# Kernel tuning notes

Hardware: AMD Instinct MI355X
Metric: run time of the kernel (lower is better)

## Reference

```python
import jax, jax.numpy as jnp
import numpy as np

N_NODES = 100000
N_SUPPORTS = 3
N_EDGES = 500000
D_IN = 128
D_OUT = 128


def setup_inputs() -> dict:
    key = jax.random.key(0)
    k1, k2, k3, k4, k5 = jax.random.split(key, 5)
    x = jax.random.normal(k1, (N_NODES, D_IN), dtype=jnp.float32)
    # glorot-ish scale for weights
    W = jax.random.normal(k2, (N_SUPPORTS, D_IN, D_OUT), dtype=jnp.float32) * np.sqrt(2.0 / (D_IN + D_OUT)).astype(np.float32)
    edge_src = jax.random.randint(k3, (N_SUPPORTS, N_EDGES), 0, N_NODES, dtype=jnp.int32)
    edge_dst = jax.random.randint(k4, (N_SUPPORTS, N_EDGES), 0, N_NODES, dtype=jnp.int32)
    edge_val = jax.random.uniform(k5, (N_SUPPORTS, N_EDGES), dtype=jnp.float32)
    return {"x": x, "W": W, "edge_src": edge_src, "edge_dst": edge_dst, "edge_val": edge_val}


def reference(x, W, edge_src, edge_dst, edge_val):
    """HMGConvolution forward (adj_power=1, multi_weight, no attention/reweight).

    x:        [N, Din] dense node features
    W:        [S, Din, Dout] per-support weights
    edge_src: [S, E] source node ids of each adjacency (COO)
    edge_dst: [S, E] destination node ids
    edge_val: [S, E] adjacency values
    Returns relu(sum_s  A_s @ (x @ W_s))  -> [N, Dout]
    """
    n_nodes = x.shape[0]
    # dense transform per support: [S, N, Dout]
    pre_sup = jnp.einsum('nd,sde->sne', x, W)

    def spmm(pre_s, src, dst, val):
        # messages gathered from source nodes, scaled by edge weight
        msgs = val[:, None] * pre_s[src]  # [E, Dout]
        return jax.ops.segment_sum(msgs, dst, num_segments=n_nodes)  # [N, Dout]

    supports = jax.vmap(spmm)(pre_sup, edge_src, edge_dst, edge_val)  # [S, N, Dout]
    return jax.nn.relu(jnp.sum(supports, axis=0))
```

## Files before the change

### kernel.cpp

```cpp
#include <hip/hip_runtime.h>

#define DIN 128
#define DOUT 128
#define EPB 4096
#define BKT 512
#define PACK_BITS 19
#define SRCG_MASK ((1u << PACK_BITS) - 1u)

typedef __attribute__((ext_vector_type(8))) short short8;
typedef __attribute__((ext_vector_type(4))) float f32x4;
typedef __attribute__((ext_vector_type(8))) unsigned short ushort8;

__device__ __forceinline__ unsigned short f2bf(float f) {
  unsigned int u = __float_as_uint(f);
  u += 0x7fffu + ((u >> 16) & 1u);
  return (unsigned short)(u >> 16);
}


__global__ __launch_bounds__(256) void gemm_mfma(const float* __restrict__ x,
                                                 const float* __restrict__ W,
                                                 unsigned short* __restrict__ pre,
                                                 int n_nodes, int n_sup) {
  __shared__ unsigned short xs[128][136];
  __shared__ unsigned short wt[128][136];

  const int tid = threadIdx.x;
  const int lane = tid & 63;
  const int w = tid >> 6;
  const int row0 = blockIdx.x * 128;
  const int alr = lane & 15;
  const int akg = lane >> 4;

#pragma unroll
  for (int i = 0; i < 16; ++i) {
    int e = tid + i * 256;
    int r = e >> 5;
    int c = (e & 31) * 4;
    int gr = row0 + r;
    float4 v = make_float4(0.f, 0.f, 0.f, 0.f);
    if (gr < n_nodes) v = *reinterpret_cast<const float4*>(&x[(size_t)gr * DIN + c]);
    xs[r][c] = f2bf(v.x); xs[r][c + 1] = f2bf(v.y);
    xs[r][c + 2] = f2bf(v.z); xs[r][c + 3] = f2bf(v.w);
  }
  __syncthreads();

  short8 afrag[4][2];
#pragma unroll
  for (int kc = 0; kc < 4; ++kc)
#pragma unroll
    for (int mt = 0; mt < 2; ++mt)
      afrag[kc][mt] = *reinterpret_cast<const short8*>(
          &xs[w * 32 + mt * 16 + alr][kc * 32 + akg * 8]);

  for (int s = 0; s < n_sup; ++s) {
    const float* Ws = W + (size_t)s * DIN * DOUT;
    __syncthreads();
#pragma unroll
    for (int i = 0; i < 16; ++i) {
      int e = tid + i * 256;
      int k = e >> 5;
      int c = (e & 31) * 4;
      float4 v = *reinterpret_cast<const float4*>(&Ws[(size_t)k * DOUT + c]);
      wt[c][k] = f2bf(v.x); wt[c + 1][k] = f2bf(v.y);
      wt[c + 2][k] = f2bf(v.z); wt[c + 3][k] = f2bf(v.w);
    }
    __syncthreads();

    f32x4 acc[2][8];
#pragma unroll
    for (int mt = 0; mt < 2; ++mt)
#pragma unroll
      for (int nt = 0; nt < 8; ++nt) acc[mt][nt] = (f32x4){0.f, 0.f, 0.f, 0.f};

#pragma unroll
    for (int kc = 0; kc < 4; ++kc) {
      short8 bfrag[8];
#pragma unroll
      for (int nt = 0; nt < 8; ++nt)
        bfrag[nt] = *reinterpret_cast<const short8*>(
            &wt[nt * 16 + alr][kc * 32 + akg * 8]);
#pragma unroll
      for (int mt = 0; mt < 2; ++mt)
#pragma unroll
        for (int nt = 0; nt < 8; ++nt)
          acc[mt][nt] = __builtin_amdgcn_mfma_f32_16x16x32_bf16(
              afrag[kc][mt], bfrag[nt], acc[mt][nt], 0, 0, 0);
    }
    __syncthreads();

#pragma unroll
    for (int mt = 0; mt < 2; ++mt)
#pragma unroll
      for (int nt = 0; nt < 8; ++nt)
#pragma unroll
        for (int q = 0; q < 4; ++q)
          wt[w * 32 + mt * 16 + akg * 4 + q][nt * 16 + alr] = f2bf(acc[mt][nt][q]);
    __syncthreads();

    unsigned short* ps = pre + (size_t)s * n_nodes * DOUT;
#pragma unroll
    for (int i = 0; i < 8; ++i) {
      int e = tid + i * 256;
      int r = e >> 4;
      int c = (e & 15) * 8;
      int gr = row0 + r;
      if (gr < n_nodes)
        *reinterpret_cast<ushort8*>(&ps[(size_t)gr * DOUT + c]) =
            *reinterpret_cast<const ushort8*>(&wt[r][c]);
    }
  }
}


__global__ __launch_bounds__(256) void gemm_xw(const float* __restrict__ x,
                                               const float* __restrict__ W,
                                               float* __restrict__ pre,
                                               int n_nodes) {
  __shared__ float xsf[128][33];
  __shared__ float wtf[32][129];
  const float* Ws = W + (size_t)blockIdx.y * DIN * DOUT;
  float* pres = pre + (size_t)blockIdx.y * n_nodes * DOUT;
  const int tid = threadIdx.x;
  const int row0 = blockIdx.x * 128;
  const int tcol = tid & 15;
  const int trow = tid >> 4;
  float acc[8][8];
#pragma unroll
  for (int i = 0; i < 8; ++i)
#pragma unroll
    for (int j = 0; j < 8; ++j) acc[i][j] = 0.f;
#pragma unroll 1
  for (int kk = 0; kk < DIN; kk += 32) {
#pragma unroll
    for (int i = 0; i < 4; ++i) {
      int e = tid + i * 256;
      int r = e >> 3, c = (e & 7) * 4;
      int gr = row0 + r;
      float4 v = make_float4(0.f, 0.f, 0.f, 0.f);
      if (gr < n_nodes)
        v = *reinterpret_cast<const float4*>(&x[(size_t)gr * DIN + kk + c]);
      xsf[r][c] = v.x; xsf[r][c + 1] = v.y; xsf[r][c + 2] = v.z; xsf[r][c + 3] = v.w;
    }
#pragma unroll
    for (int i = 0; i < 4; ++i) {
      int e = tid + i * 256;
      int k = e >> 5, c = (e & 31) * 4;
      float4 v = *reinterpret_cast<const float4*>(&Ws[(size_t)(kk + k) * DOUT + c]);
      wtf[k][c] = v.x; wtf[k][c + 1] = v.y; wtf[k][c + 2] = v.z; wtf[k][c + 3] = v.w;
    }
    __syncthreads();
#pragma unroll 4
    for (int k = 0; k < 32; ++k) {
      float a[8], b[8];
#pragma unroll
      for (int i = 0; i < 8; ++i) a[i] = xsf[trow * 8 + i][k];
#pragma unroll
      for (int j = 0; j < 8; ++j) b[j] = wtf[k][tcol + 16 * j];
#pragma unroll
      for (int i = 0; i < 8; ++i)
#pragma unroll
        for (int j = 0; j < 8; ++j) acc[i][j] = fmaf(a[i], b[j], acc[i][j]);
    }
    __syncthreads();
  }
#pragma unroll
  for (int i = 0; i < 8; ++i) {
    int gr = row0 + trow * 8 + i;
    if (gr < n_nodes) {
#pragma unroll
      for (int j = 0; j < 8; ++j)
        pres[(size_t)gr * DOUT + tcol + 16 * j] = acc[i][j];
    }
  }
}


__global__ __launch_bounds__(256) void bucket_count(const int* __restrict__ dst_all,
                                                    int* __restrict__ bucket_cnt, int TE) {
  __shared__ int cnt[256];
  const int tid = threadIdx.x;
  cnt[tid] = 0;
  __syncthreads();
  const int beg = blockIdx.x * EPB;
  const int end = min(beg + EPB, TE);
  for (int i = beg + tid; i < end; i += 256) atomicAdd(&cnt[dst_all[i] >> 9], 1);
  __syncthreads();
  int c = cnt[tid];
  if (c) atomicAdd(&bucket_cnt[tid], c);
}

__global__ __launch_bounds__(256) void bucket_scan(const int* __restrict__ bucket_cnt,
                                                   int* __restrict__ bucket_base,
                                                   int* __restrict__ bucket_cursor,
                                                   int NB, int TE) {
  __shared__ int tmp[256];
  const int tid = threadIdx.x;
  int v = (tid < NB) ? bucket_cnt[tid] : 0;
  tmp[tid] = v;
  __syncthreads();
#pragma unroll
  for (int d = 1; d < 256; d <<= 1) {
    int t = (tid >= d) ? tmp[tid - d] : 0;
    __syncthreads();
    tmp[tid] += t;
    __syncthreads();
  }
  int excl = tmp[tid] - v;
  if (tid < NB) {
    bucket_base[tid] = excl;
    bucket_cursor[tid] = excl;
  }
  if (tid == 0) bucket_base[NB] = TE;
}

__global__ __launch_bounds__(256) void partition_edges(const int* __restrict__ src_all,
                                                       const int* __restrict__ dst_all,
                                                       const float* __restrict__ val_all,
                                                       int* __restrict__ bucket_cursor,
                                                       int2* __restrict__ part,
                                                       int TE, int n_nodes, int n_edges) {
  __shared__ int cnt[256];
  __shared__ int base_l[256];
  const int tid = threadIdx.x;
  const int beg = blockIdx.x * EPB;
  const int end = min(beg + EPB, TE);

  cnt[tid] = 0;
  __syncthreads();
  for (int i = beg + tid; i < end; i += 256) atomicAdd(&cnt[dst_all[i] >> 9], 1);
  __syncthreads();

  int c = cnt[tid];
  int mybase = (c > 0) ? atomicAdd(&bucket_cursor[tid], c) : 0;
  __syncthreads();
  base_l[tid] = mybase;
  cnt[tid] = 0;
  __syncthreads();

  for (int i = beg + tid; i < end; i += 256) {
    int d = dst_all[i];
    int b = d >> 9;
    int r = atomicAdd(&cnt[b], 1);
    int s = i / n_edges;
    unsigned key = (unsigned)(s * n_nodes + src_all[i]) |
                   ((unsigned)(d & (BKT - 1)) << PACK_BITS);
    part[base_l[b] + r] = make_int2((int)key, __float_as_int(val_all[i]));
  }
}

__global__ __launch_bounds__(256) void csr_build(const int2* __restrict__ part,
                                                 const int* __restrict__ bucket_base,
                                                 int2* __restrict__ csr,
                                                 int* __restrict__ row_off,
                                                 int n_nodes, int TE) {
  __shared__ int cnt[BKT];
  __shared__ int off_s[BKT];
  __shared__ int tmp[256];
  const int b = blockIdx.x;
  const int tid = threadIdx.x;
  const int bb = bucket_base[b];
  const int be = bucket_base[b + 1];

  cnt[tid] = 0;
  cnt[tid + 256] = 0;
  __syncthreads();
  for (int j = bb + tid; j < be; j += 256)
    atomicAdd(&cnt[((unsigned)part[j].x) >> PACK_BITS], 1);
  __syncthreads();

  int s2 = cnt[2 * tid] + cnt[2 * tid + 1];
  tmp[tid] = s2;
  __syncthreads();
#pragma unroll
  for (int d = 1; d < 256; d <<= 1) {
    int t = (tid >= d) ? tmp[tid - d] : 0;
    __syncthreads();
    tmp[tid] += t;
    __syncthreads();
  }
  int excl2 = tmp[tid] - s2;
  off_s[2 * tid] = excl2;
  off_s[2 * tid + 1] = excl2 + cnt[2 * tid];
  __syncthreads();

#pragma unroll
  for (int k = tid; k < BKT; k += 256) {
    int node = b * BKT + k;
    if (node < n_nodes) row_off[node] = bb + off_s[k];
  }
  cnt[tid] = off_s[tid];
  cnt[tid + 256] = off_s[tid + 256];
  __syncthreads();

  for (int j = bb + tid; j < be; j += 256) {
    int2 e = part[j];
    int dl = ((unsigned)e.x) >> PACK_BITS;
    int p = bb + atomicAdd(&cnt[dl], 1);
    csr[p] = e;
  }
  if (b == 0 && tid == 0) row_off[n_nodes] = TE;
}


__global__ __launch_bounds__(256) void spmm_gather8(const unsigned short* __restrict__ pre,
                                                    const int2* __restrict__ csr,
                                                    const int* __restrict__ row_off,
                                                    float* __restrict__ out, int n_nodes) {
  const int lane = threadIdx.x & 63;
  const int g = lane >> 3;
  const int t = lane & 7;
  const int wave = blockIdx.x * (blockDim.x >> 6) + (threadIdx.x >> 6);
  const int nwaves = gridDim.x * (blockDim.x >> 6);

  for (int n = wave; n < n_nodes; n += nwaves) {
    const int beg = row_off[n];
    const int end = row_off[n + 1];
    float acc[16];
#pragma unroll
    for (int k = 0; k < 16; ++k) acc[k] = 0.f;

    for (int j = beg + g; j < end; j += 8) {
      const int2 e = csr[j];
      const float v = __int_as_float(e.y);
      const unsigned srcg = ((unsigned)e.x) & SRCG_MASK;
      const ushort8* pr =
          reinterpret_cast<const ushort8*>(&pre[(size_t)srcg * DOUT + t * 16]);
      ushort8 p0 = pr[0];
      ushort8 p1 = pr[1];
#pragma unroll
      for (int k = 0; k < 8; ++k) {
        acc[k]     = fmaf(v, __uint_as_float((unsigned int)(unsigned short)p0[k] << 16), acc[k]);
        acc[8 + k] = fmaf(v, __uint_as_float((unsigned int)(unsigned short)p1[k] << 16), acc[8 + k]);
      }
    }

#pragma unroll
    for (int d = 8; d <= 32; d <<= 1)
#pragma unroll
      for (int k = 0; k < 16; ++k) acc[k] += __shfl_xor(acc[k], d, 64);

    float r0 = 0.f, r1 = 0.f;
#pragma unroll
    for (int gg = 0; gg < 8; ++gg)
      if (gg == g) { r0 = acc[gg * 2]; r1 = acc[gg * 2 + 1]; }
    r0 = fmaxf(r0, 0.f);
    r1 = fmaxf(r1, 0.f);
    *reinterpret_cast<float2*>(&out[(size_t)n * DOUT + t * 16 + g * 2]) =
        make_float2(r0, r1);
  }
}


__global__ __launch_bounds__(256) void edge_hist(const int* __restrict__ dst_base,
                                                 int* __restrict__ counts,
                                                 int n_edges, int n_nodes) {
  int i = blockIdx.x * blockDim.x + threadIdx.x;
  int s = blockIdx.y;
  if (i < n_edges) atomicAdd(&counts[s * n_nodes + dst_base[(size_t)s * n_edges + i]], 1);
}

__global__ __launch_bounds__(256) void scan_local(const int* __restrict__ counts,
                                                  int* __restrict__ row_off,
                                                  int* __restrict__ partials, int n) {
  __shared__ int tmp[256];
  const int tid = threadIdx.x;
  const int base = blockIdx.x * 2048 + tid * 8;
  int v[8];
#pragma unroll
  for (int i = 0; i < 8; ++i) v[i] = (base + i < n) ? counts[base + i] : 0;
  int s = 0;
#pragma unroll
  for (int i = 0; i < 8; ++i) s += v[i];
  tmp[tid] = s;
  __syncthreads();
#pragma unroll
  for (int d = 1; d < 256; d <<= 1) {
    int t = (tid >= d) ? tmp[tid - d] : 0;
    __syncthreads();
    tmp[tid] += t;
    __syncthreads();
  }
  int p = tmp[tid] - s;
#pragma unroll
  for (int i = 0; i < 8; ++i) {
    if (base + i < n) row_off[base + i] = p;
    p += v[i];
  }
  if (tid == 255) partials[blockIdx.x] = tmp[255];
}

__global__ __launch_bounds__(256) void scan_partials_k(int* __restrict__ partials, int nblk) {
  __shared__ int tmp[256];
  const int tid = threadIdx.x;
  int v = (tid < nblk) ? partials[tid] : 0;
  tmp[tid] = v;
  __syncthreads();
#pragma unroll
  for (int d = 1; d < 256; d <<= 1) {
    int t = (tid >= d) ? tmp[tid - d] : 0;
    __syncthreads();
    tmp[tid] += t;
    __syncthreads();
  }
  if (tid < nblk) partials[tid] = tmp[tid] - v;
}

__global__ __launch_bounds__(256) void scan_finish(int* __restrict__ row_off,
                                                   int* __restrict__ cursor,
                                                   const int* __restrict__ partials,
                                                   int n, int total_edges) {
  const int off = partials[blockIdx.x];
  const int base = blockIdx.x * 2048 + threadIdx.x * 8;
#pragma unroll
  for (int i = 0; i < 8; ++i) {
    int idx = base + i;
    if (idx < n) {
      int v = row_off[idx] + off;
      row_off[idx] = v;
      cursor[idx] = v;
    }
  }
  if (blockIdx.x == 0 && threadIdx.x == 0) row_off[n] = total_edges;
}

__global__ __launch_bounds__(256) void edge_fill(const int* __restrict__ src_base,
                                                 const int* __restrict__ dst_base,
                                                 const float* __restrict__ val_base,
                                                 int* __restrict__ cursor,
                                                 int2* __restrict__ csr,
                                                 int n_edges, int n_nodes) {
  int i = blockIdx.x * blockDim.x + threadIdx.x;
  int s = blockIdx.y;
  if (i < n_edges) {
    size_t gi = (size_t)s * n_edges + i;
    int d = dst_base[gi];
    int pos = atomicAdd(&cursor[s * n_nodes + d], 1);
    csr[pos] = make_int2(src_base[gi], __float_as_int(val_base[gi]));
  }
}

__global__ __launch_bounds__(256) void spmm_gather(const float* __restrict__ pre,
                                                   const int2* __restrict__ csr,
                                                   const int* __restrict__ row_off,
                                                   float* __restrict__ out,
                                                   int n_nodes, int n_sup, int mode) {
  const int lane = threadIdx.x & 63;
  const int wave = blockIdx.x * (blockDim.x >> 6) + (threadIdx.x >> 6);
  const int nwaves = gridDim.x * (blockDim.x >> 6);
  for (int n = wave; n < n_nodes; n += nwaves) {
    float ax = 0.f, ay = 0.f;
    float2* o = reinterpret_cast<float2*>(&out[(size_t)n * DOUT + lane * 2]);
    if (mode & 1) { float2 prev = *o; ax = prev.x; ay = prev.y; }
    for (int s = 0; s < n_sup; ++s) {
      const float* ps = pre + (size_t)s * n_nodes * DOUT;
      const int row = s * n_nodes + n;
      const int beg = row_off[row];
      const int end = row_off[row + 1];
      for (int j = beg; j < end; ++j) {
        const int2 e = csr[j];
        const float v = __int_as_float(e.y);
        const float2 p = *reinterpret_cast<const float2*>(&ps[(size_t)e.x * DOUT + lane * 2]);
        ax = fmaf(v, p.x, ax);
        ay = fmaf(v, p.y, ay);
      }
    }
    if (mode & 2) { ax = fmaxf(ax, 0.f); ay = fmaxf(ay, 0.f); }
    *o = make_float2(ax, ay);
  }
}

__global__ __launch_bounds__(256) void zero_f4(float4* __restrict__ p, int n4) {
  int i = blockIdx.x * blockDim.x + threadIdx.x;
  int stride = gridDim.x * blockDim.x;
  float4 z = make_float4(0.f, 0.f, 0.f, 0.f);
  for (; i < n4; i += stride) p[i] = z;
}

__global__ __launch_bounds__(256) void relu_f4(float4* __restrict__ p, int n4) {
  int i = blockIdx.x * blockDim.x + threadIdx.x;
  int stride = gridDim.x * blockDim.x;
  for (; i < n4; i += stride) {
    float4 v = p[i];
    v.x = fmaxf(v.x, 0.f); v.y = fmaxf(v.y, 0.f);
    v.z = fmaxf(v.z, 0.f); v.w = fmaxf(v.w, 0.f);
    p[i] = v;
  }
}

__global__ __launch_bounds__(256) void spmm_atomic(const float* __restrict__ pre,
                                                   const int* __restrict__ src,
                                                   const int* __restrict__ dst,
                                                   const float* __restrict__ val,
                                                   float* __restrict__ out,
                                                   int n_edges) {
  const int lane = threadIdx.x & 63;
  const int wave = blockIdx.x * (blockDim.x >> 6) + (threadIdx.x >> 6);
  const int nwaves = gridDim.x * (blockDim.x >> 6);
  for (int e = wave; e < n_edges; e += nwaves) {
    int s = src[e];
    int d = dst[e];
    float v = val[e];
    const float2 p = *reinterpret_cast<const float2*>(&pre[(size_t)s * DOUT + lane * 2]);
    float* o = &out[(size_t)d * DOUT + lane * 2];
    atomicAdd(o, v * p.x);
    atomicAdd(o + 1, v * p.y);
  }
}


static inline size_t align_up(size_t v, size_t a) { return (v + a - 1) & ~(a - 1); }

extern "C" void kernel_launch(void* const* d_in, const int* in_sizes, int n_in,
                              void* d_out, int out_size, void* d_ws, size_t ws_size,
                              hipStream_t stream) {
  const float* x     = (const float*)d_in[0];
  const float* W     = (const float*)d_in[1];
  const int*   esrc  = (const int*)d_in[2];
  const int*   edst  = (const int*)d_in[3];
  const float* eval_ = (const float*)d_in[4];
  float* out = (float*)d_out;

  const int n_nodes    = in_sizes[0] / DIN;
  const int n_supports = in_sizes[1] / (DIN * DOUT);
  const int n_edges    = in_sizes[2] / n_supports;

  const int gemm_blocks = (n_nodes + 127) / 128;
  const int edge_blocks = (n_edges + 255) / 256;
  const int gather_blocks = (n_nodes + 3) / 4;

  {
    const int NR = n_supports * n_nodes;
    const int TE = n_supports * n_edges;
    const int NB = (n_nodes + BKT - 1) / BKT;
    const int eb = (TE + EPB - 1) / EPB;
    char* w = (char*)d_ws;
    size_t off = 0;
    unsigned short* pre3 = (unsigned short*)(w + off); off += align_up((size_t)NR * DOUT * 2, 256);
    int* row_off = (int*)(w + off);      off += align_up((size_t)(n_nodes + 1) * 4, 256);
    int2* part = (int2*)(w + off);       off += align_up((size_t)TE * 8, 256);
    int2* csr = (int2*)(w + off);        off += align_up((size_t)TE * 8, 256);
    int* bucket_cnt = (int*)(w + off);   off += align_up(256 * 4, 256);
    int* bucket_base = (int*)(w + off);  off += align_up(257 * 4, 256);
    int* bucket_cur = (int*)(w + off);   off += align_up(256 * 4, 256);

    const bool packable = (size_t)n_supports * n_nodes < (1u << PACK_BITS);

    if (off <= ws_size && NB <= 256 && packable) {
      gemm_mfma<<<gemm_blocks, 256, 0, stream>>>(x, W, pre3, n_nodes, n_supports);
      hipMemsetAsync(bucket_cnt, 0, 256 * 4, stream);
      bucket_count<<<eb, 256, 0, stream>>>(edst, bucket_cnt, TE);
      bucket_scan<<<1, 256, 0, stream>>>(bucket_cnt, bucket_base, bucket_cur, NB, TE);
      partition_edges<<<eb, 256, 0, stream>>>(esrc, edst, eval_, bucket_cur, part,
                                              TE, n_nodes, n_edges);
      csr_build<<<NB, 256, 0, stream>>>(part, bucket_base, csr, row_off, n_nodes, TE);
      spmm_gather8<<<gather_blocks, 256, 0, stream>>>(pre3, csr, row_off, out, n_nodes);
      return;
    }
  }

  {
    const int scan_blocks = (n_nodes + 2047) / 2048;
    char* w = (char*)d_ws;
    size_t off = 0;
    float* pre = (float*)(w + off);    off += align_up((size_t)n_nodes * DOUT * 4, 256);
    int* row_off = (int*)(w + off);    off += align_up((size_t)(n_nodes + 1) * 4, 256);
    int* cursor = (int*)(w + off);     off += align_up((size_t)n_nodes * 4, 256);
    int2* csr = (int2*)(w + off);      off += align_up((size_t)n_edges * 8, 256);
    int* partials = (int*)(w + off);   off += align_up(1024 * 4, 256);

    if (off <= ws_size && scan_blocks <= 256) {
      for (int s = 0; s < n_supports; ++s) {
        const int* src = esrc + (size_t)s * n_edges;
        const int* dst = edst + (size_t)s * n_edges;
        const float* val = eval_ + (size_t)s * n_edges;
        gemm_xw<<<dim3(gemm_blocks, 1), 256, 0, stream>>>(x, W + (size_t)s * DIN * DOUT,
                                                          pre, n_nodes);
        hipMemsetAsync(cursor, 0, (size_t)n_nodes * 4, stream);
        edge_hist<<<dim3(edge_blocks, 1), 256, 0, stream>>>(dst, cursor, n_edges, n_nodes);
        scan_local<<<scan_blocks, 256, 0, stream>>>(cursor, row_off, partials, n_nodes);
        scan_partials_k<<<1, 256, 0, stream>>>(partials, scan_blocks);
        scan_finish<<<scan_blocks, 256, 0, stream>>>(row_off, cursor, partials, n_nodes, n_edges);
        edge_fill<<<dim3(edge_blocks, 1), 256, 0, stream>>>(src, dst, val, cursor, csr,
                                                            n_edges, n_nodes);
        int mode = (s == 0) ? 0 : 1;
        if (s == n_supports - 1) mode |= 2;
        spmm_gather<<<gather_blocks, 256, 0, stream>>>(pre, csr, row_off, out,
                                                       n_nodes, 1, mode);
      }
      return;
    }
  }

  {
    float* pre = (float*)d_ws;
    if (ws_size < (size_t)n_nodes * DOUT * 4) return;
    const int n4 = out_size / 4;
    zero_f4<<<2048, 256, 0, stream>>>((float4*)out, n4);
    for (int s = 0; s < n_supports; ++s) {
      gemm_xw<<<dim3(gemm_blocks, 1), 256, 0, stream>>>(x, W + (size_t)s * DIN * DOUT,
                                                        pre, n_nodes);
      spmm_atomic<<<2048, 256, 0, stream>>>(pre, esrc + (size_t)s * n_edges,
                                            edst + (size_t)s * n_edges,
                                            eval_ + (size_t)s * n_edges, out, n_edges);
    }
    relu_f4<<<2048, 256, 0, stream>>>((float4*)out, n4);
  }
}
```

Baseline: 200.3 us.

## Pre-convert W to transposed bf16 once and load GEMM fragments from global

A new small kernel converts each support's weight matrix to bf16 and transposes it once, so GEMM blocks no longer convert and transpose W into shared memory for every support. The GEMM now builds its A fragments straight from global fp32 x in registers and reads B fragments from the pre-transposed bf16 buffer in global memory (served from cache). This removes the per-block shared staging, most barriers, and one LDS buffer, which may raise occupancy. In exchange it adds an extra kernel launch and relies on L2/L1 hits for repeated B fragment loads.

```diff
diff --git a/kernel.cpp b/kernel.cpp
--- a/kernel.cpp
+++ b/kernel.cpp
@@ -18,12 +18,37 @@
 }
 
 
+__global__ __launch_bounds__(256) void wconvert(const float* __restrict__ W,
+                                                unsigned short* __restrict__ wT) {
+  __shared__ unsigned short buf[128][136];
+  const int s = blockIdx.x;
+  const float* Ws = W + (size_t)s * DIN * DOUT;
+  unsigned short* wts = wT + (size_t)s * DIN * DOUT;
+  const int tid = threadIdx.x;
+#pragma unroll
+  for (int i = 0; i < 16; ++i) {
+    int e = tid + i * 256;
+    int k = e >> 5, c = (e & 31) * 4;
+    float4 v = *reinterpret_cast<const float4*>(&Ws[(size_t)k * DOUT + c]);
+    buf[c][k] = f2bf(v.x); buf[c + 1][k] = f2bf(v.y);
+    buf[c + 2][k] = f2bf(v.z); buf[c + 3][k] = f2bf(v.w);
+  }
+  __syncthreads();
+#pragma unroll
+  for (int i = 0; i < 8; ++i) {
+    int e = tid + i * 256;
+    int r = e >> 4, c = (e & 15) * 8;
+    *reinterpret_cast<ushort8*>(&wts[(size_t)r * DIN + c]) =
+        *reinterpret_cast<const ushort8*>(&buf[r][c]);
+  }
+}
+
+
 __global__ __launch_bounds__(256) void gemm_mfma(const float* __restrict__ x,
-                                                 const float* __restrict__ W,
+                                                 const unsigned short* __restrict__ wT,
                                                  unsigned short* __restrict__ pre,
                                                  int n_nodes, int n_sup) {
-  __shared__ unsigned short xs[128][136];
-  __shared__ unsigned short wt[128][136];
+  __shared__ unsigned short cst[128][136];
 
   const int tid = threadIdx.x;
   const int lane = tid & 63;
@@ -32,40 +57,28 @@
   const int alr = lane & 15;
   const int akg = lane >> 4;
 
-#pragma unroll
-  for (int i = 0; i < 16; ++i) {
-    int e = tid + i * 256;
-    int r = e >> 5;
-    int c = (e & 31) * 4;
-    int gr = row0 + r;
-    float4 v = make_float4(0.f, 0.f, 0.f, 0.f);
-    if (gr < n_nodes) v = *reinterpret_cast<const float4*>(&x[(size_t)gr * DIN + c]);
-    xs[r][c] = f2bf(v.x); xs[r][c + 1] = f2bf(v.y);
-    xs[r][c + 2] = f2bf(v.z); xs[r][c + 3] = f2bf(v.w);
-  }
-  __syncthreads();
-
   short8 afrag[4][2];
 #pragma unroll
   for (int kc = 0; kc < 4; ++kc)
 #pragma unroll
-    for (int mt = 0; mt < 2; ++mt)
-      afrag[kc][mt] = *reinterpret_cast<const short8*>(
-          &xs[w * 32 + mt * 16 + alr][kc * 32 + akg * 8]);
+    for (int mt = 0; mt < 2; ++mt) {
+      int gr = row0 + w * 32 + mt * 16 + alr;
+      short8 a = {0, 0, 0, 0, 0, 0, 0, 0};
+      if (gr < n_nodes) {
+        const float4* p =
+            reinterpret_cast<const float4*>(&x[(size_t)gr * DIN + kc * 32 + akg * 8]);
+        float4 v0 = p[0];
+        float4 v1 = p[1];
+        a[0] = (short)f2bf(v0.x); a[1] = (short)f2bf(v0.y);
+        a[2] = (short)f2bf(v0.z); a[3] = (short)f2bf(v0.w);
+        a[4] = (short)f2bf(v1.x); a[5] = (short)f2bf(v1.y);
+        a[6] = (short)f2bf(v1.z); a[7] = (short)f2bf(v1.w);
+      }
+      afrag[kc][mt] = a;
+    }
 
   for (int s = 0; s < n_sup; ++s) {
-    const float* Ws = W + (size_t)s * DIN * DOUT;
-    __syncthreads();
-#pragma unroll
-    for (int i = 0; i < 16; ++i) {
-      int e = tid + i * 256;
-      int k = e >> 5;
-      int c = (e & 31) * 4;
-      float4 v = *reinterpret_cast<const float4*>(&Ws[(size_t)k * DOUT + c]);
-      wt[c][k] = f2bf(v.x); wt[c + 1][k] = f2bf(v.y);
-      wt[c + 2][k] = f2bf(v.z); wt[c + 3][k] = f2bf(v.w);
-    }
-    __syncthreads();
+    const unsigned short* wts = wT + (size_t)s * DIN * DOUT;
 
     f32x4 acc[2][8];
 #pragma unroll
@@ -79,7 +92,7 @@
 #pragma unroll
       for (int nt = 0; nt < 8; ++nt)
         bfrag[nt] = *reinterpret_cast<const short8*>(
-            &wt[nt * 16 + alr][kc * 32 + akg * 8]);
+            &wts[(size_t)(nt * 16 + alr) * DIN + kc * 32 + akg * 8]);
 #pragma unroll
       for (int mt = 0; mt < 2; ++mt)
 #pragma unroll
@@ -87,15 +100,15 @@
           acc[mt][nt] = __builtin_amdgcn_mfma_f32_16x16x32_bf16(
               afrag[kc][mt], bfrag[nt], acc[mt][nt], 0, 0, 0);
     }
-    __syncthreads();
-
+
+    __syncthreads();
 #pragma unroll
     for (int mt = 0; mt < 2; ++mt)
 #pragma unroll
       for (int nt = 0; nt < 8; ++nt)
 #pragma unroll
         for (int q = 0; q < 4; ++q)
-          wt[w * 32 + mt * 16 + akg * 4 + q][nt * 16 + alr] = f2bf(acc[mt][nt][q]);
+          cst[w * 32 + mt * 16 + akg * 4 + q][nt * 16 + alr] = f2bf(acc[mt][nt][q]);
     __syncthreads();
 
     unsigned short* ps = pre + (size_t)s * n_nodes * DOUT;
@@ -107,7 +120,7 @@
       int gr = row0 + r;
       if (gr < n_nodes)
         *reinterpret_cast<ushort8*>(&ps[(size_t)gr * DOUT + c]) =
-            *reinterpret_cast<const ushort8*>(&wt[r][c]);
+            *reinterpret_cast<const ushort8*>(&cst[r][c]);
     }
   }
 }
@@ -537,6 +550,7 @@
     char* w = (char*)d_ws;
     size_t off = 0;
     unsigned short* pre3 = (unsigned short*)(w + off); off += align_up((size_t)NR * DOUT * 2, 256);
+    unsigned short* wT = (unsigned short*)(w + off);   off += align_up((size_t)n_supports * DIN * DOUT * 2, 256);
     int* row_off = (int*)(w + off);      off += align_up((size_t)(n_nodes + 1) * 4, 256);
     int2* part = (int2*)(w + off);       off += align_up((size_t)TE * 8, 256);
     int2* csr = (int2*)(w + off);        off += align_up((size_t)TE * 8, 256);
@@ -547,7 +561,8 @@
     const bool packable = (size_t)n_supports * n_nodes < (1u << PACK_BITS);
 
     if (off <= ws_size && NB <= 256 && packable) {
-      gemm_mfma<<<gemm_blocks, 256, 0, stream>>>(x, W, pre3, n_nodes, n_supports);
+      wconvert<<<n_supports, 256, 0, stream>>>(W, wT);
+      gemm_mfma<<<gemm_blocks, 256, 0, stream>>>(x, wT, pre3, n_nodes, n_supports);
       hipMemsetAsync(bucket_cnt, 0, 256 * 4, stream);
       bucket_count<<<eb, 256, 0, stream>>>(edst, bucket_cnt, TE);
       bucket_scan<<<1, 256, 0, stream>>>(bucket_cnt, bucket_base, bucket_cur, NB, TE);
```

Measured after the change: 190.2 us. 5.1% less time.
